# Optimization experiments

Measured on AMD Instinct MI355X. Metric: run time of the kernel, lower is better.

The kernel has to match this reference:

```python
import jax, jax.numpy as jnp
import numpy as np

DISCARD_RATIO = 0.9  # AttentionRollout default
TOP_K_RATIO = 0.1
NUM_HEADS = 12


def _rollout(attn_hist):
    """Attention rollout. attn_hist: [L, B, H, N, N] -> CLS scores [B, N-1]."""
    L, B, H, N, _ = attn_hist.shape
    keep = N - int(N * DISCARD_RATIO)  # complement of discarded smallest entries
    eye = jnp.eye(N, dtype=attn_hist.dtype)
    bi = jnp.arange(B)[:, None, None]
    ri = jnp.arange(N)[None, :, None]

    def step(result, attn):
        fused = attn.mean(axis=1)  # head fusion 'mean' -> [B, N, N]
        _, idx = jax.lax.top_k(fused, keep)  # keep largest == discard smallest
        mask = jnp.zeros_like(fused).at[bi, ri, idx].set(1.0)
        mask = mask.at[:, :, 0].set(1.0)  # always keep CLS column
        a = fused * mask
        a = (a + eye[None]) * 0.5  # residual: 0.5*S + 0.5*I
        a = a / a.sum(axis=-1, keepdims=True)
        return jnp.einsum('bij,bjk->bik', a, result), None

    res0 = jnp.tile(eye[None], (B, 1, 1))
    result, _ = jax.lax.scan(step, res0, attn_hist)
    return result[:, 0, 1:]  # CLS attention to patches


def setup_inputs() -> dict:
    key = jax.random.key(0)
    ks = jax.random.split(key, 10)
    B, N, C, H, L = 4, 577, 768, 12, 12
    x = jax.random.normal(ks[0], (B, N, C), jnp.float32)
    # realistic attention maps: rows are softmax distributions
    attention_history = jax.nn.softmax(
        jax.random.normal(ks[1], (L, B, H, N, N), jnp.float32), axis=-1)
    w = 0.02
    return {
        'x': x,
        'attention_history': attention_history,
        'Wq': jax.random.normal(ks[2], (C, C), jnp.float32) * w,
        'bq': jnp.zeros((C,), jnp.float32),
        'Wk': jax.random.normal(ks[3], (C, C), jnp.float32) * w,
        'bk': jnp.zeros((C,), jnp.float32),
        'Wv': jax.random.normal(ks[4], (C, C), jnp.float32) * w,
        'bv': jnp.zeros((C,), jnp.float32),
        'Wo': jax.random.normal(ks[5], (C, C), jnp.float32) * w,
        'bo': jnp.zeros((C,), jnp.float32),
    }


def reference(x, attention_history, Wq, bq, Wk, bk, Wv, bv, Wo, bo):
    B, N, C = x.shape
    H = NUM_HEADS
    D = C // H
    scale = D ** -0.5

    # rollout (no-grad in torch) -> select top-k local queries
    scores = jax.lax.stop_gradient(_rollout(attention_history))  # [B, N-1]
    num_sel = max(1, int((N - 1) * TOP_K_RATIO))
    _, sel = jax.lax.top_k(scores, num_sel)
    sel = sel + 1  # shift past CLS token

    # global K/V from all tokens
    k = (x @ Wk.T + bk).reshape(B, N, H, D).transpose(0, 2, 1, 3)  # [B,H,N,D]
    v = (x @ Wv.T + bv).reshape(B, N, H, D).transpose(0, 2, 1, 3)

    # local queries gathered at selected patches
    lq = jnp.take_along_axis(x, sel[:, :, None], axis=1)  # [B,S,C]
    q = (lq @ Wq.T + bq).reshape(B, num_sel, H, D).transpose(0, 2, 1, 3)

    attn = jnp.einsum('bhsd,bhnd->bhsn', q, k) * scale
    attn_w = jax.nn.softmax(attn, axis=-1)  # [B,H,S,N]
    out = jnp.einsum('bhsn,bhnd->bhsd', attn_w, v)
    out = out.transpose(0, 2, 1, 3).reshape(B, num_sel, C)
    out = out @ Wo.T + bo

    # scatter: CLS copied, selected positions get attended features,
    # positions not selected in ANY batch copy x, others remain zero
    bi = jnp.arange(B)[:, None]
    output = jnp.zeros_like(x).at[:, 0].set(x[:, 0]).at[bi, sel].set(out)
    sel_union = jnp.zeros((N,), bool).at[sel.reshape(-1)].set(True)
    non_sel = (jnp.arange(N) != 0) & (~sel_union)
    output = jnp.where(non_sel[None, :, None], x, output)
    return output, attn_w
```

## Files before the change

kernel.cpp:

```cpp
#include <hip/hip_runtime.h>

#define NTOK 577
#define BATCH 4
#define HEADS 12
#define LAYERS 12
#define CDIM 768
#define SSEL 57
#define KEEP 58
#define MROWS (BATCH * NTOK)
#define NR 10
#define IC 16

__global__ void init_kernel(int* selpos, int* unionmask) {
  int i = blockIdx.x * 256 + threadIdx.x;
  if (i < BATCH * NTOK) selpos[i] = 0;
  if (i < NTOK) unionmask[i] = 0;
}

__global__ __launch_bounds__(256) void fuse_all(const float* __restrict__ ah,
                                                float* __restrict__ Abuf) {
  const int w = blockIdx.x * 4 + (threadIdx.x >> 6);
  const int lane = threadIdx.x & 63;
  const int l = w / (BATCH * NTOK);
  const int rr = w % (BATCH * NTOK);
  const int b = rr / NTOK;
  const int i = rr % NTOK;
  const float* base =
      ah + ((((size_t)l * BATCH + b) * HEADS) * NTOK + i) * NTOK;

  float val[NR];
  unsigned ub[NR];
#pragma unroll
  for (int r = 0; r < NR; ++r) {
    const int j = lane + 64 * r;
    float s = 0.f;
    if (j < NTOK) {
#pragma unroll
      for (int h = 0; h < HEADS; ++h)
        s += __builtin_nontemporal_load(&base[(size_t)h * NTOK * NTOK + j]);
      s = s / 12.f;
    }
    val[r] = s;
    ub[r] = (j < NTOK) ? __float_as_uint(s) : 0u;
  }

  unsigned tau = 0u;
  for (int bit = 30; bit >= 0; --bit) {
    const unsigned cand = tau | (1u << bit);
    int c = 0;
#pragma unroll
    for (int r = 0; r < NR; ++r) c += ((ub[r] >> bit) >= (cand >> bit));
#pragma unroll
    for (int off = 1; off < 64; off <<= 1) c += __shfl_xor(c, off, 64);
    if (c >= KEEP) tau = cand;
  }

  int cgt = 0;
#pragma unroll
  for (int r = 0; r < NR; ++r) cgt += (ub[r] > tau);
#pragma unroll
  for (int off = 1; off < 64; off <<= 1) cgt += __shfl_xor(cgt, off, 64);
  const int keq = KEEP - cgt;

  unsigned long long em[NR];
#pragma unroll
  for (int r = 0; r < NR; ++r) em[r] = __ballot(ub[r] == tau);
  const unsigned long long ltm = (1ull << lane) - 1ull;

  bool kp[NR];
  int pre = 0;
  float ksum = 0.f;
#pragma unroll
  for (int r = 0; r < NR; ++r) {
    const int j = lane + 64 * r;
    bool k1 = (ub[r] > tau);
    if (ub[r] == tau) {
      const int rank = pre + __popcll(em[r] & ltm);
      k1 = (rank < keq);
    }
    if (j == 0) k1 = true;
    kp[r] = k1;
    if (k1) ksum += val[r];
    pre += __popcll(em[r]);
  }
#pragma unroll
  for (int off = 1; off < 64; off <<= 1) ksum += __shfl_xor(ksum, off, 64);
  const float inv = 1.f / (ksum + 1.f);

  float* Arow = Abuf + (((size_t)(l * BATCH + b) * NTOK) + i) * NTOK;
#pragma unroll
  for (int r = 0; r < NR; ++r) {
    const int j = lane + 64 * r;
    if (j < NTOK)
      Arow[j] = ((kp[r] ? val[r] : 0.f) + ((j == i) ? 1.f : 0.f)) * inv;
  }
}

__global__ __launch_bounds__(256) void vmul_part(const float* __restrict__ Al,
                                                 const float* __restrict__ pin,
                                                 float* __restrict__ pout) {
  const int b = blockIdx.x / 3;
  const int jc = blockIdx.x % 3;
  const int ic = blockIdx.y;
  const int tid = threadIdx.x;
  __shared__ float vsh[NTOK];
  for (int t = tid; t < NTOK; t += 256) {
    float s;
    if (pin) {
      s = 0.f;
#pragma unroll
      for (int c = 0; c < IC; ++c) s += pin[c * MROWS + b * NTOK + t];
    } else {
      s = (t == 0) ? 1.f : 0.f;
    }
    vsh[t] = s;
  }
  __syncthreads();
  const int j = jc * 256 + tid;
  if (j >= NTOK) return;
  const int i0 = ic * 36;
  const int i1 = (ic == IC - 1) ? NTOK : (i0 + 36);
  const float* Ab = Al + (size_t)b * NTOK * NTOK + j;
  float acc = 0.f;
  for (int i = i0; i < i1; ++i) acc += vsh[i] * Ab[(size_t)i * NTOK];
  pout[ic * MROWS + b * NTOK + j] = acc;
}

__global__ __launch_bounds__(64) void topk_kernel(const float* __restrict__ pin,
                                                  int* __restrict__ sel,
                                                  int* __restrict__ selpos,
                                                  int* __restrict__ unionmask,
                                                  int* __restrict__ rowidx) {
  const int b = blockIdx.x;
  const int lane = threadIdx.x;
  unsigned long long key[NR];
#pragma unroll
  for (int r = 0; r < NR; ++r) {
    const int n = lane + 64 * r;
    unsigned long long k2 = 0ull;
    if (n >= 1 && n < NTOK) {
      float s = 0.f;
#pragma unroll
      for (int c = 0; c < IC; ++c) s += pin[c * MROWS + b * NTOK + n];
      k2 = (((unsigned long long)__float_as_uint(s)) << 32) |
           (unsigned long long)(0xFFFFFFFFu - (unsigned)n);
    }
    key[r] = k2;
  }
  for (int s = 0; s < SSEL; ++s) {
    unsigned long long mk = 0ull;
#pragma unroll
    for (int r = 0; r < NR; ++r) mk = (key[r] > mk) ? key[r] : mk;
#pragma unroll
    for (int off = 1; off < 64; off <<= 1) {
      unsigned long long o = __shfl_xor(mk, off, 64);
      if (o > mk) mk = o;
    }
    const int n = (int)(0xFFFFFFFFu - (unsigned)(mk & 0xFFFFFFFFull));
#pragma unroll
    for (int r = 0; r < NR; ++r)
      if (key[r] == mk) key[r] = 0ull;
    if (lane == 0) {
      sel[b * SSEL + s] = n;
      selpos[b * NTOK + n] = s + 1;
      unionmask[n] = 1;
      rowidx[b * SSEL + s] = b * NTOK + n;
    }
  }
}

__global__ __launch_bounds__(256) void gemm_nt(const float* __restrict__ A,
                                               const float* __restrict__ W,
                                               const float* __restrict__ bias,
                                               float* __restrict__ C, int M,
                                               const int* __restrict__ rowidx) {
  __shared__ float As[16][68];
  __shared__ float Bs[16][68];
  const int tid = threadIdx.x;
  const int lm = tid >> 2;
  const int lk = (tid & 3) << 2;
  const int mrow = blockIdx.x * 64 + lm;
  const bool mv = (mrow < M);
  const float* Abase = A;
  if (mv) {
    int ridx = rowidx ? rowidx[mrow] : mrow;
    Abase = A + (size_t)ridx * CDIM;
  }
  const int nrow = blockIdx.y * 64 + lm;
  const float* Wbase = W + (size_t)nrow * CDIM;

  const int m0 = (tid & 15) << 2;
  const int n0 = (tid >> 4) << 2;
  float acc[4][4] = {{0.f}};

  for (int k0 = 0; k0 < CDIM; k0 += 16) {
    float4 av = mv ? *(const float4*)(Abase + k0 + lk) : make_float4(0.f, 0.f, 0.f, 0.f);
    float4 bv = *(const float4*)(Wbase + k0 + lk);
    __syncthreads();
    As[lk + 0][lm] = av.x; As[lk + 1][lm] = av.y;
    As[lk + 2][lm] = av.z; As[lk + 3][lm] = av.w;
    Bs[lk + 0][lm] = bv.x; Bs[lk + 1][lm] = bv.y;
    Bs[lk + 2][lm] = bv.z; Bs[lk + 3][lm] = bv.w;
    __syncthreads();
#pragma unroll
    for (int k = 0; k < 16; ++k) {
      float a0 = As[k][m0 + 0], a1 = As[k][m0 + 1], a2 = As[k][m0 + 2], a3 = As[k][m0 + 3];
      float b0 = Bs[k][n0 + 0], b1 = Bs[k][n0 + 1], b2 = Bs[k][n0 + 2], b3 = Bs[k][n0 + 3];
      acc[0][0] += a0 * b0; acc[0][1] += a0 * b1; acc[0][2] += a0 * b2; acc[0][3] += a0 * b3;
      acc[1][0] += a1 * b0; acc[1][1] += a1 * b1; acc[1][2] += a1 * b2; acc[1][3] += a1 * b3;
      acc[2][0] += a2 * b0; acc[2][1] += a2 * b1; acc[2][2] += a2 * b2; acc[2][3] += a2 * b3;
      acc[3][0] += a3 * b0; acc[3][1] += a3 * b1; acc[3][2] += a3 * b2; acc[3][3] += a3 * b3;
    }
  }
  const int cmBase = blockIdx.x * 64 + m0;
  const int cnBase = blockIdx.y * 64 + n0;
#pragma unroll
  for (int ii = 0; ii < 4; ++ii) {
    int cm = cmBase + ii;
    if (cm < M) {
      float* crow = C + (size_t)cm * CDIM + cnBase;
#pragma unroll
      for (int jj = 0; jj < 4; ++jj) crow[jj] = acc[ii][jj] + bias[cnBase + jj];
    }
  }
}

__global__ __launch_bounds__(256) void attn_kernel(const float* __restrict__ qbuf,
                                                   const float* __restrict__ kbuf,
                                                   const float* __restrict__ vbuf,
                                                   float* __restrict__ attnw,
                                                   float* __restrict__ obuf) {
  const int bx = blockIdx.x;
  const int b = bx / (HEADS * 8);
  const int rem = bx % (HEADS * 8);
  const int h = rem / 8;
  const int ch = rem % 8;
  const int s0 = ch * 8;
  int ns = SSEL - s0;
  if (ns > 8) ns = 8;
  const int tid = threadIdx.x;
  __shared__ float Q[8][64];
  __shared__ float P[8][580];
  __shared__ float sred[4];
  __shared__ float sbc;

  for (int t = tid; t < 512; t += 256) {
    int s = t >> 6, d = t & 63;
    Q[s][d] = (s < ns) ? qbuf[((size_t)(b * SSEL + s0 + s)) * CDIM + h * 64 + d] : 0.f;
  }
  __syncthreads();

  for (int e = tid; e < ns * NTOK; e += 256) {
    int s = e / NTOK, n = e % NTOK;
    const float* kr = kbuf + ((size_t)(b * NTOK + n)) * CDIM + h * 64;
    float acc = 0.f;
#pragma unroll
    for (int d = 0; d < 64; ++d) acc += Q[s][d] * kr[d];
    P[s][n] = acc * 0.125f;
  }
  __syncthreads();

  for (int s = 0; s < ns; ++s) {
    float m = -1e30f;
    for (int n = tid; n < NTOK; n += 256) m = fmaxf(m, P[s][n]);
    for (int off = 32; off; off >>= 1) m = fmaxf(m, __shfl_down(m, off, 64));
    if ((tid & 63) == 0) sred[tid >> 6] = m;
    __syncthreads();
    if (tid == 0) sbc = fmaxf(fmaxf(sred[0], sred[1]), fmaxf(sred[2], sred[3]));
    __syncthreads();
    m = sbc;
    float lsum = 0.f;
    for (int n = tid; n < NTOK; n += 256) {
      float e_ = expf(P[s][n] - m);
      P[s][n] = e_;
      lsum += e_;
    }
    for (int off = 32; off; off >>= 1) lsum += __shfl_down(lsum, off, 64);
    if ((tid & 63) == 0) sred[tid >> 6] = lsum;
    __syncthreads();
    if (tid == 0) sbc = 1.f / (sred[0] + sred[1] + sred[2] + sred[3]);
    __syncthreads();
    float inv = sbc;
    float* aw = attnw + ((size_t)((b * HEADS + h) * SSEL + s0 + s)) * NTOK;
    for (int n = tid; n < NTOK; n += 256) {
      float p = P[s][n] * inv;
      P[s][n] = p;
      aw[n] = p;
    }
    __syncthreads();
  }

  for (int t = tid; t < ns * 64; t += 256) {
    int s = t >> 6, d = t & 63;
    float acc = 0.f;
    for (int n = 0; n < NTOK; ++n)
      acc += P[s][n] * vbuf[((size_t)(b * NTOK + n)) * CDIM + h * 64 + d];
    obuf[((size_t)(b * SSEL + s0 + s)) * CDIM + h * 64 + d] = acc;
  }
}

__global__ void scatter_kernel(const float* __restrict__ x, const float* __restrict__ o2,
                               const int* __restrict__ selpos,
                               const int* __restrict__ unionmask,
                               float* __restrict__ out) {
  int idx = blockIdx.x * 256 + threadIdx.x;
  const int total = BATCH * NTOK * CDIM;
  if (idx >= total) return;
  int b = idx / (NTOK * CDIM);
  int r = idx % (NTOK * CDIM);
  int n = r / CDIM;
  int c = r % CDIM;
  float val;
  if (n == 0) {
    val = x[idx];
  } else {
    int sp = selpos[b * NTOK + n];
    if (sp > 0)
      val = o2[((size_t)(b * SSEL + sp - 1)) * CDIM + c];
    else if (unionmask[n])
      val = 0.f;
    else
      val = x[idx];
  }
  out[idx] = val;
}

extern "C" void kernel_launch(void* const* d_in, const int* in_sizes, int n_in,
                              void* d_out, int out_size, void* d_ws, size_t ws_size,
                              hipStream_t stream) {
  const float* x = (const float*)d_in[0];
  const float* ah = (const float*)d_in[1];
  const float* Wq = (const float*)d_in[2];
  const float* bq = (const float*)d_in[3];
  const float* Wk = (const float*)d_in[4];
  const float* bk = (const float*)d_in[5];
  const float* Wv = (const float*)d_in[6];
  const float* bv = (const float*)d_in[7];
  const float* Wo = (const float*)d_in[8];
  const float* bo = (const float*)d_in[9];
  float* out = (float*)d_out;
  float* attnw = out + (size_t)BATCH * NTOK * CDIM;

  char* w = (char*)d_ws;
  auto carve = [&](size_t bytes) -> char* {
    char* p = w;
    w += (bytes + 255) & ~(size_t)255;
    return p;
  };
  float* Abuf = (float*)carve((size_t)LAYERS * BATCH * NTOK * NTOK * 4);
  float* partA = (float*)carve((size_t)IC * MROWS * 4);
  float* partB = (float*)carve((size_t)IC * MROWS * 4);
  float* kbuf = (float*)carve((size_t)MROWS * CDIM * 4);
  float* vbuf = (float*)carve((size_t)MROWS * CDIM * 4);
  float* qbuf = (float*)carve((size_t)BATCH * SSEL * CDIM * 4);
  float* obuf = (float*)carve((size_t)BATCH * SSEL * CDIM * 4);
  float* o2buf = (float*)carve((size_t)BATCH * SSEL * CDIM * 4);
  int* selbuf = (int*)carve((size_t)BATCH * SSEL * 4);
  int* selpos = (int*)carve((size_t)BATCH * NTOK * 4);
  int* unionm = (int*)carve((size_t)NTOK * 4);
  int* rowidx = (int*)carve((size_t)BATCH * SSEL * 4);

  init_kernel<<<(BATCH * NTOK + 255) / 256, 256, 0, stream>>>(selpos, unionm);

  fuse_all<<<(LAYERS * MROWS) / 4, 256, 0, stream>>>(ah, Abuf);

  const float* pin = nullptr;
  float* pout = partA;
  for (int t = 0; t < LAYERS; ++t) {
    int l = LAYERS - 1 - t;
    vmul_part<<<dim3(BATCH * 3, IC), 256, 0, stream>>>(
        Abuf + (size_t)l * BATCH * NTOK * NTOK, pin, pout);
    pin = pout;
    pout = (pout == partA) ? partB : partA;
  }
  topk_kernel<<<BATCH, 64, 0, stream>>>(pin, selbuf, selpos, unionm, rowidx);

  dim3 gKV((MROWS + 63) / 64, CDIM / 64);
  gemm_nt<<<gKV, 256, 0, stream>>>(x, Wk, bk, kbuf, MROWS, nullptr);
  gemm_nt<<<gKV, 256, 0, stream>>>(x, Wv, bv, vbuf, MROWS, nullptr);
  dim3 gQ((BATCH * SSEL + 63) / 64, CDIM / 64);
  gemm_nt<<<gQ, 256, 0, stream>>>(x, Wq, bq, qbuf, BATCH * SSEL, rowidx);
  attn_kernel<<<BATCH * HEADS * 8, 256, 0, stream>>>(qbuf, kbuf, vbuf, attnw, obuf);
  gemm_nt<<<gQ, 256, 0, stream>>>(obuf, Wo, bo, o2buf, BATCH * SSEL, nullptr);
  scatter_kernel<<<(BATCH * NTOK * CDIM + 255) / 256, 256, 0, stream>>>(
      x, o2buf, selpos, unionm, out);
}
```

Baseline: 1.715 ms.

## Merge init, K/V GEMMs and head fusion into one launch; persistent rollout chain

Folds the init kernel, the K and V projection GEMM tiles and the head-fusion pass into a single heterogeneous launch, so the compute-bound GEMM tiles can share the GPU with the bandwidth-bound fusion blocks. The twelve vector-matrix rollout launches and the top-k launch become one persistent kernel that separates layers with atomic grid barriers. This cuts launch count and lets independent work overlap. The risk is that the spin-wait barrier depends on all 192 blocks being resident at once, and the barrier counters are reset by the previous launch.

Measured after the change: 1.866 ms. 1.09x slower.

```diff
diff --git a/kernel.cpp b/kernel.cpp
--- a/kernel.cpp
+++ b/kernel.cpp
@@ -11,16 +11,103 @@
 #define NR 10
 #define IC 16
 
-__global__ void init_kernel(int* selpos, int* unionmask) {
-  int i = blockIdx.x * 256 + threadIdx.x;
-  if (i < BATCH * NTOK) selpos[i] = 0;
-  if (i < NTOK) unionmask[i] = 0;
-}
-
-__global__ __launch_bounds__(256) void fuse_all(const float* __restrict__ ah,
-                                                float* __restrict__ Abuf) {
-  const int w = blockIdx.x * 4 + (threadIdx.x >> 6);
-  const int lane = threadIdx.x & 63;
+#define NINIT 10
+#define NKVT ((MROWS + 63) / 64)
+#define NKV (2 * NKVT * (CDIM / 64))
+#define NFUSE (LAYERS * MROWS / 4)
+#define NB_CHAIN (BATCH * 3 * IC)
+
+__device__ __forceinline__ void gemm_tile(int bx, int by,
+                                          const float* __restrict__ A,
+                                          const float* __restrict__ W,
+                                          const float* __restrict__ bias,
+                                          float* __restrict__ C, int M,
+                                          const int* __restrict__ rowidx,
+                                          float (*As)[68], float (*Bs)[68]) {
+  const int tid = threadIdx.x;
+  const int lm = tid >> 2;
+  const int lk = (tid & 3) << 2;
+  const int mrow = bx * 64 + lm;
+  const bool mv = (mrow < M);
+  const float* Abase = A;
+  if (mv) {
+    int ridx = rowidx ? rowidx[mrow] : mrow;
+    Abase = A + (size_t)ridx * CDIM;
+  }
+  const int nrow = by * 64 + lm;
+  const float* Wbase = W + (size_t)nrow * CDIM;
+
+  const int m0 = (tid & 15) << 2;
+  const int n0 = (tid >> 4) << 2;
+  float acc[4][4] = {{0.f}};
+
+  for (int k0 = 0; k0 < CDIM; k0 += 16) {
+    float4 av = mv ? *(const float4*)(Abase + k0 + lk) : make_float4(0.f, 0.f, 0.f, 0.f);
+    float4 bv = *(const float4*)(Wbase + k0 + lk);
+    __syncthreads();
+    As[lk + 0][lm] = av.x; As[lk + 1][lm] = av.y;
+    As[lk + 2][lm] = av.z; As[lk + 3][lm] = av.w;
+    Bs[lk + 0][lm] = bv.x; Bs[lk + 1][lm] = bv.y;
+    Bs[lk + 2][lm] = bv.z; Bs[lk + 3][lm] = bv.w;
+    __syncthreads();
+#pragma unroll
+    for (int k = 0; k < 16; ++k) {
+      float a0 = As[k][m0 + 0], a1 = As[k][m0 + 1], a2 = As[k][m0 + 2], a3 = As[k][m0 + 3];
+      float b0 = Bs[k][n0 + 0], b1 = Bs[k][n0 + 1], b2 = Bs[k][n0 + 2], b3 = Bs[k][n0 + 3];
+      acc[0][0] += a0 * b0; acc[0][1] += a0 * b1; acc[0][2] += a0 * b2; acc[0][3] += a0 * b3;
+      acc[1][0] += a1 * b0; acc[1][1] += a1 * b1; acc[1][2] += a1 * b2; acc[1][3] += a1 * b3;
+      acc[2][0] += a2 * b0; acc[2][1] += a2 * b1; acc[2][2] += a2 * b2; acc[2][3] += a2 * b3;
+      acc[3][0] += a3 * b0; acc[3][1] += a3 * b1; acc[3][2] += a3 * b2; acc[3][3] += a3 * b3;
+    }
+  }
+  const int cmBase = bx * 64 + m0;
+  const int cnBase = by * 64 + n0;
+#pragma unroll
+  for (int ii = 0; ii < 4; ++ii) {
+    int cm = cmBase + ii;
+    if (cm < M) {
+      float* crow = C + (size_t)cm * CDIM + cnBase;
+#pragma unroll
+      for (int jj = 0; jj < 4; ++jj) crow[jj] = acc[ii][jj] + bias[cnBase + jj];
+    }
+  }
+}
+
+__global__ __launch_bounds__(256) void mega1(
+    const float* __restrict__ ah, float* __restrict__ Abuf,
+    const float* __restrict__ x, const float* __restrict__ Wk,
+    const float* __restrict__ bk, float* __restrict__ kbuf,
+    const float* __restrict__ Wv, const float* __restrict__ bv,
+    float* __restrict__ vbuf, int* __restrict__ selpos,
+    int* __restrict__ unionm, int* __restrict__ barcnt) {
+  __shared__ float As[16][68];
+  __shared__ float Bs[16][68];
+  const int bx = blockIdx.x;
+  const int tid = threadIdx.x;
+
+  if (bx < NINIT) {
+    int i = bx * 256 + tid;
+    if (i < MROWS) selpos[i] = 0;
+    if (i < NTOK) unionm[i] = 0;
+    if (i < 16) barcnt[i] = 0;
+    return;
+  }
+
+  if (bx < NINIT + NKV) {
+    const int idx = bx - NINIT;
+    const int which = idx / (NKV / 2);
+    const int r = idx % (NKV / 2);
+    const int gx = r % NKVT;
+    const int gy = r / NKVT;
+    if (which == 0)
+      gemm_tile(gx, gy, x, Wk, bk, kbuf, MROWS, nullptr, As, Bs);
+    else
+      gemm_tile(gx, gy, x, Wv, bv, vbuf, MROWS, nullptr, As, Bs);
+    return;
+  }
+
+  const int w = (bx - NINIT - NKV) * 4 + (tid >> 6);
+  const int lane = tid & 63;
   const int l = w / (BATCH * NTOK);
   const int rr = w % (BATCH * NTOK);
   const int b = rr / NTOK;
@@ -96,75 +183,95 @@
   }
 }
 
-__global__ __launch_bounds__(256) void vmul_part(const float* __restrict__ Al,
-                                                 const float* __restrict__ pin,
-                                                 float* __restrict__ pout) {
-  const int b = blockIdx.x / 3;
-  const int jc = blockIdx.x % 3;
-  const int ic = blockIdx.y;
+__device__ __forceinline__ void grid_barrier(int* cnt, int nb) {
+  __syncthreads();
+  if (threadIdx.x == 0) {
+    __hip_atomic_fetch_add(cnt, 1, __ATOMIC_RELEASE, __HIP_MEMORY_SCOPE_AGENT);
+    while (__hip_atomic_load(cnt, __ATOMIC_RELAXED, __HIP_MEMORY_SCOPE_AGENT) < nb)
+      __builtin_amdgcn_s_sleep(2);
+  }
+  __syncthreads();
+  __threadfence();
+}
+
+__global__ __launch_bounds__(256) void chain_kernel(
+    const float* __restrict__ Abuf, float* __restrict__ partA,
+    float* __restrict__ partB, int* __restrict__ barcnt,
+    int* __restrict__ sel, int* __restrict__ selpos,
+    int* __restrict__ unionm, int* __restrict__ rowidx) {
+  const int blk = blockIdx.x;
   const int tid = threadIdx.x;
+  const int ic = blk / 12;
+  const int rem = blk % 12;
+  const int b = rem / 3;
+  const int jc = rem % 3;
   __shared__ float vsh[NTOK];
-  for (int t = tid; t < NTOK; t += 256) {
-    float s;
-    if (pin) {
-      s = 0.f;
-#pragma unroll
-      for (int c = 0; c < IC; ++c) s += pin[c * MROWS + b * NTOK + t];
-    } else {
-      s = (t == 0) ? 1.f : 0.f;
-    }
-    vsh[t] = s;
-  }
-  __syncthreads();
   const int j = jc * 256 + tid;
-  if (j >= NTOK) return;
   const int i0 = ic * 36;
   const int i1 = (ic == IC - 1) ? NTOK : (i0 + 36);
-  const float* Ab = Al + (size_t)b * NTOK * NTOK + j;
-  float acc = 0.f;
-  for (int i = i0; i < i1; ++i) acc += vsh[i] * Ab[(size_t)i * NTOK];
-  pout[ic * MROWS + b * NTOK + j] = acc;
-}
-
-__global__ __launch_bounds__(64) void topk_kernel(const float* __restrict__ pin,
-                                                  int* __restrict__ sel,
-                                                  int* __restrict__ selpos,
-                                                  int* __restrict__ unionmask,
-                                                  int* __restrict__ rowidx) {
-  const int b = blockIdx.x;
-  const int lane = threadIdx.x;
-  unsigned long long key[NR];
-#pragma unroll
-  for (int r = 0; r < NR; ++r) {
-    const int n = lane + 64 * r;
-    unsigned long long k2 = 0ull;
-    if (n >= 1 && n < NTOK) {
-      float s = 0.f;
-#pragma unroll
-      for (int c = 0; c < IC; ++c) s += pin[c * MROWS + b * NTOK + n];
-      k2 = (((unsigned long long)__float_as_uint(s)) << 32) |
-           (unsigned long long)(0xFFFFFFFFu - (unsigned)n);
-    }
-    key[r] = k2;
-  }
-  for (int s = 0; s < SSEL; ++s) {
-    unsigned long long mk = 0ull;
-#pragma unroll
-    for (int r = 0; r < NR; ++r) mk = (key[r] > mk) ? key[r] : mk;
-#pragma unroll
-    for (int off = 1; off < 64; off <<= 1) {
-      unsigned long long o = __shfl_xor(mk, off, 64);
-      if (o > mk) mk = o;
-    }
-    const int n = (int)(0xFFFFFFFFu - (unsigned)(mk & 0xFFFFFFFFull));
-#pragma unroll
-    for (int r = 0; r < NR; ++r)
-      if (key[r] == mk) key[r] = 0ull;
-    if (lane == 0) {
-      sel[b * SSEL + s] = n;
-      selpos[b * NTOK + n] = s + 1;
-      unionmask[n] = 1;
-      rowidx[b * SSEL + s] = b * NTOK + n;
+
+  for (int t = 0; t < LAYERS; ++t) {
+    const int l = LAYERS - 1 - t;
+    const float* pin = (t == 0) ? nullptr : ((t & 1) ? partA : partB);
+    float* pout = (t & 1) ? partB : partA;
+    for (int tt = tid; tt < NTOK; tt += 256) {
+      float s;
+      if (pin) {
+        s = 0.f;
+#pragma unroll
+        for (int c = 0; c < IC; ++c) s += pin[c * MROWS + b * NTOK + tt];
+      } else {
+        s = (tt == 0) ? 1.f : 0.f;
+      }
+      vsh[tt] = s;
+    }
+    __syncthreads();
+    if (j < NTOK) {
+      const float* Ab =
+          Abuf + (size_t)l * BATCH * NTOK * NTOK + (size_t)b * NTOK * NTOK + j;
+      float acc = 0.f;
+      for (int i = i0; i < i1; ++i) acc += vsh[i] * Ab[(size_t)i * NTOK];
+      pout[ic * MROWS + b * NTOK + j] = acc;
+    }
+    grid_barrier(&barcnt[t], NB_CHAIN);
+  }
+
+  if (blk < BATCH && tid < 64) {
+    const int bb = blk;
+    const int lane = tid;
+    unsigned long long key[NR];
+#pragma unroll
+    for (int r = 0; r < NR; ++r) {
+      const int n = lane + 64 * r;
+      unsigned long long k2 = 0ull;
+      if (n >= 1 && n < NTOK) {
+        float s = 0.f;
+#pragma unroll
+        for (int c = 0; c < IC; ++c) s += partB[c * MROWS + bb * NTOK + n];
+        k2 = (((unsigned long long)__float_as_uint(s)) << 32) |
+             (unsigned long long)(0xFFFFFFFFu - (unsigned)n);
+      }
+      key[r] = k2;
+    }
+    for (int s = 0; s < SSEL; ++s) {
+      unsigned long long mk = 0ull;
+#pragma unroll
+      for (int r = 0; r < NR; ++r) mk = (key[r] > mk) ? key[r] : mk;
+#pragma unroll
+      for (int off = 1; off < 64; off <<= 1) {
+        unsigned long long o = __shfl_xor(mk, off, 64);
+        if (o > mk) mk = o;
+      }
+      const int n = (int)(0xFFFFFFFFu - (unsigned)(mk & 0xFFFFFFFFull));
+#pragma unroll
+      for (int r = 0; r < NR; ++r)
+        if (key[r] == mk) key[r] = 0ull;
+      if (lane == 0) {
+        sel[bb * SSEL + s] = n;
+        selpos[bb * NTOK + n] = s + 1;
+        unionm[n] = 1;
+        rowidx[bb * SSEL + s] = bb * NTOK + n;
+      }
     }
   }
 }
@@ -176,53 +283,7 @@
                                                const int* __restrict__ rowidx) {
   __shared__ float As[16][68];
   __shared__ float Bs[16][68];
-  const int tid = threadIdx.x;
-  const int lm = tid >> 2;
-  const int lk = (tid & 3) << 2;
-  const int mrow = blockIdx.x * 64 + lm;
-  const bool mv = (mrow < M);
-  const float* Abase = A;
-  if (mv) {
-    int ridx = rowidx ? rowidx[mrow] : mrow;
-    Abase = A + (size_t)ridx * CDIM;
-  }
-  const int nrow = blockIdx.y * 64 + lm;
-  const float* Wbase = W + (size_t)nrow * CDIM;
-
-  const int m0 = (tid & 15) << 2;
-  const int n0 = (tid >> 4) << 2;
-  float acc[4][4] = {{0.f}};
-
-  for (int k0 = 0; k0 < CDIM; k0 += 16) {
-    float4 av = mv ? *(const float4*)(Abase + k0 + lk) : make_float4(0.f, 0.f, 0.f, 0.f);
-    float4 bv = *(const float4*)(Wbase + k0 + lk);
-    __syncthreads();
-    As[lk + 0][lm] = av.x; As[lk + 1][lm] = av.y;
-    As[lk + 2][lm] = av.z; As[lk + 3][lm] = av.w;
-    Bs[lk + 0][lm] = bv.x; Bs[lk + 1][lm] = bv.y;
-    Bs[lk + 2][lm] = bv.z; Bs[lk + 3][lm] = bv.w;
-    __syncthreads();
-#pragma unroll
-    for (int k = 0; k < 16; ++k) {
-      float a0 = As[k][m0 + 0], a1 = As[k][m0 + 1], a2 = As[k][m0 + 2], a3 = As[k][m0 + 3];
-      float b0 = Bs[k][n0 + 0], b1 = Bs[k][n0 + 1], b2 = Bs[k][n0 + 2], b3 = Bs[k][n0 + 3];
-      acc[0][0] += a0 * b0; acc[0][1] += a0 * b1; acc[0][2] += a0 * b2; acc[0][3] += a0 * b3;
-      acc[1][0] += a1 * b0; acc[1][1] += a1 * b1; acc[1][2] += a1 * b2; acc[1][3] += a1 * b3;
-      acc[2][0] += a2 * b0; acc[2][1] += a2 * b1; acc[2][2] += a2 * b2; acc[2][3] += a2 * b3;
-      acc[3][0] += a3 * b0; acc[3][1] += a3 * b1; acc[3][2] += a3 * b2; acc[3][3] += a3 * b3;
-    }
-  }
-  const int cmBase = blockIdx.x * 64 + m0;
-  const int cnBase = blockIdx.y * 64 + n0;
-#pragma unroll
-  for (int ii = 0; ii < 4; ++ii) {
-    int cm = cmBase + ii;
-    if (cm < M) {
-      float* crow = C + (size_t)cm * CDIM + cnBase;
-#pragma unroll
-      for (int jj = 0; jj < 4; ++jj) crow[jj] = acc[ii][jj] + bias[cnBase + jj];
-    }
-  }
+  gemm_tile(blockIdx.x, blockIdx.y, A, W, bias, C, M, rowidx, As, Bs);
 }
 
 __global__ __launch_bounds__(256) void attn_kernel(const float* __restrict__ qbuf,
@@ -359,25 +420,14 @@
   int* selpos = (int*)carve((size_t)BATCH * NTOK * 4);
   int* unionm = (int*)carve((size_t)NTOK * 4);
   int* rowidx = (int*)carve((size_t)BATCH * SSEL * 4);
-
-  init_kernel<<<(BATCH * NTOK + 255) / 256, 256, 0, stream>>>(selpos, unionm);
-
-  fuse_all<<<(LAYERS * MROWS) / 4, 256, 0, stream>>>(ah, Abuf);
-
-  const float* pin = nullptr;
-  float* pout = partA;
-  for (int t = 0; t < LAYERS; ++t) {
-    int l = LAYERS - 1 - t;
-    vmul_part<<<dim3(BATCH * 3, IC), 256, 0, stream>>>(
-        Abuf + (size_t)l * BATCH * NTOK * NTOK, pin, pout);
-    pin = pout;
-    pout = (pout == partA) ? partB : partA;
-  }
-  topk_kernel<<<BATCH, 64, 0, stream>>>(pin, selbuf, selpos, unionm, rowidx);
-
-  dim3 gKV((MROWS + 63) / 64, CDIM / 64);
-  gemm_nt<<<gKV, 256, 0, stream>>>(x, Wk, bk, kbuf, MROWS, nullptr);
-  gemm_nt<<<gKV, 256, 0, stream>>>(x, Wv, bv, vbuf, MROWS, nullptr);
+  int* barcnt = (int*)carve((size_t)16 * 4);
+
+  mega1<<<NINIT + NKV + NFUSE, 256, 0, stream>>>(
+      ah, Abuf, x, Wk, bk, kbuf, Wv, bv, vbuf, selpos, unionm, barcnt);
+
+  chain_kernel<<<NB_CHAIN, 256, 0, stream>>>(Abuf, partA, partB, barcnt,
+                                             selbuf, selpos, unionm, rowidx);
+
   dim3 gQ((BATCH * SSEL + 63) / 64, CDIM / 64);
   gemm_nt<<<gQ, 256, 0, stream>>>(x, Wq, bq, qbuf, BATCH * SSEL, rowidx);
   attn_kernel<<<BATCH * HEADS * 8, 256, 0, stream>>>(qbuf, kbuf, vbuf, attnw, obuf);
```
